# Kernel optimization log

Measured on AMD Instinct MI355X. Metric: run time of the kernel, lower is better.

Reference implementation:

```python
import jax, jax.numpy as jnp
import numpy as np

N_NODES = 100000
N_EDGES = 1000000
F_IN = 64
F_HID = 32


def setup_inputs() -> dict:
    key = jax.random.key(0)
    k = jax.random.split(key, 6)
    x = jax.random.normal(k[0], (N_NODES, F_IN), dtype=jnp.float32)
    edge_index = jax.random.randint(k[1], (2, N_EDGES), 0, N_NODES, dtype=jnp.int32)
    # Glorot-ish scaled weights (PyG GCNConv linear has no bias; bias added post-aggregation)
    W1 = jax.random.normal(k[2], (F_IN, F_HID), dtype=jnp.float32) / np.sqrt(F_IN)
    b1 = jax.random.normal(k[3], (F_HID,), dtype=jnp.float32) * 0.01
    W2 = jax.random.normal(k[4], (F_HID, F_IN), dtype=jnp.float32) / np.sqrt(F_HID)
    b2 = jax.random.normal(k[5], (F_IN,), dtype=jnp.float32) * 0.01
    return {"x": x, "edge_index": edge_index, "W1": W1, "b1": b1, "W2": W2, "b2": b2}


def gcn_conv(x, W, b, src, dst, n):
    """PyG GCNConv: h = x @ W; add self-loops; symmetric norm; scatter-add; + bias."""
    h = x @ W  # [N, out]
    ones = jnp.ones(src.shape[0], dtype=h.dtype)
    # degree includes the implicit self-loop (+1 per node)
    deg = jax.ops.segment_sum(ones, dst, num_segments=n) + 1.0  # [N]
    dis = jax.lax.rsqrt(deg)  # deg^{-1/2}
    norm = dis[src] * dis[dst]  # [E]
    agg = jax.ops.segment_sum(h[src] * norm[:, None], dst, num_segments=n)
    # self-loop contribution: norm_ii = deg_i^{-1}
    agg = agg + h * (dis * dis)[:, None]
    return agg + b


def reference(x, edge_index, W1, b1, W2, b2):
    src, dst = edge_index[0], edge_index[1]
    n = x.shape[0]
    h = jax.nn.relu(gcn_conv(x, W1, b1, src, dst, n))
    # dropout is identity in eval mode
    return gcn_conv(h, W2, b2, src, dst, n)
```

## Files before the change

kernel.cpp:

```cpp
#include <hip/hip_runtime.h>
#include <hip/hip_fp16.h>

#define NN 100000
#define NE 1000000
#define FIN 64
#define FHID 32
#define NB 782
#define BNODES 128
#define NCH 256
#define CH ((NE + NCH - 1) / NCH)
#define GEMB ((NN + 31) / 32)

union H8 { __half2 h2[4]; float4 f4; };
union H4 { __half2 h2[2]; float2 f2; };

__global__ __launch_bounds__(256) void k_bhist(const int* __restrict__ dst, int* __restrict__ phist) {
    __shared__ int lh[NB];
    for (int i = threadIdx.x; i < NB; i += 256) lh[i] = 0;
    __syncthreads();
    int k = blockIdx.x;
    int e0 = k * CH, e1 = min(e0 + CH, NE);
    for (int e = e0 + threadIdx.x; e < e1; e += 256) atomicAdd(&lh[dst[e] >> 7], 1);
    __syncthreads();
    for (int b = threadIdx.x; b < NB; b += 256) phist[(size_t)k * NB + b] = lh[b];
}

__global__ __launch_bounds__(256) void k_bscan(int* __restrict__ phist, int* __restrict__ btot) {
    int b = blockIdx.x;
    int k = threadIdx.x;
    int v = phist[(size_t)k * NB + b];
    int lane = k & 63, wv = k >> 6;
    int incl = v;
#pragma unroll
    for (int s = 1; s < 64; s <<= 1) {
        int t = __shfl_up(incl, s, 64);
        if (lane >= s) incl += t;
    }
    __shared__ int wt[4];
    if (lane == 63) wt[wv] = incl;
    __syncthreads();
    int add = 0;
#pragma unroll
    for (int w = 0; w < 4; ++w) add += (w < wv) ? wt[w] : 0;
    phist[(size_t)k * NB + b] = add + incl - v;
    if (k == 255) btot[b] = add + incl;
}

__global__ __launch_bounds__(1024) void k_bbase(const int* __restrict__ btot, int* __restrict__ bbase,
                                                int* __restrict__ off) {
    __shared__ int s[1024];
    int b = threadIdx.x;
    int v = (b < NB) ? btot[b] : 0;
    s[b] = v;
    __syncthreads();
    for (int d = 1; d < 1024; d <<= 1) {
        int t = (b >= d) ? s[b - d] : 0;
        __syncthreads();
        s[b] += t;
        __syncthreads();
    }
    if (b < NB) bbase[b] = s[b] - v;
    if (b == 0) { bbase[NB] = NE; off[NN] = NE; }
}

__global__ __launch_bounds__(256) void k_scatter_gemm1(const int* __restrict__ ei,
                                                       const int* __restrict__ phist,
                                                       const int* __restrict__ bbase,
                                                       int* __restrict__ ebuf,
                                                       const float* __restrict__ x,
                                                       const float* __restrict__ W1,
                                                       __half* __restrict__ h1) {
    int r = blockIdx.x;
    bool issc;
    int id;
    if (r < 2 * NCH) { issc = !(r & 1); id = r >> 1; }
    else             { issc = false;    id = r - NCH; }
    if (issc) {
        __shared__ int lh[NB];
        __shared__ int lbase[NB];
        int k = id;
        for (int b = threadIdx.x; b < NB; b += 256) {
            lh[b] = 0;
            lbase[b] = bbase[b] + phist[(size_t)k * NB + b];
        }
        __syncthreads();
        int e0 = k * CH, e1 = min(e0 + CH, NE);
        for (int e = e0 + threadIdx.x; e < e1; e += 256) {
            int s = ei[e], d = ei[NE + e];
            int bb = d >> 7;
            int rr = atomicAdd(&lh[bb], 1);
            ebuf[lbase[bb] + rr] = s * BNODES + (d & 127);
        }
        return;
    }
    __shared__ float Wl[FIN * FHID];
    for (int t = threadIdx.x; t < FIN * FHID / 4; t += 256)
        reinterpret_cast<float4*>(Wl)[t] = reinterpret_cast<const float4*>(W1)[t];
    __syncthreads();
    int row = id * 32 + (threadIdx.x >> 3);
    int l = threadIdx.x & 7;
    if (row >= NN) return;
    const float4* xr = reinterpret_cast<const float4*>(x + (size_t)row * FIN);
    float4 acc = make_float4(0.f, 0.f, 0.f, 0.f);
#pragma unroll
    for (int k4 = 0; k4 < FIN / 4; ++k4) {
        float4 a4 = xr[k4];
#pragma unroll
        for (int j = 0; j < 4; ++j) {
            float a = j == 0 ? a4.x : j == 1 ? a4.y : j == 2 ? a4.z : a4.w;
            const float4 wv = *reinterpret_cast<const float4*>(Wl + (k4 * 4 + j) * FHID + l * 4);
            acc.x += a * wv.x; acc.y += a * wv.y; acc.z += a * wv.z; acc.w += a * wv.w;
        }
    }
    H4 u;
    u.h2[0] = __floats2half2_rn(acc.x, acc.y);
    u.h2[1] = __floats2half2_rn(acc.z, acc.w);
    *reinterpret_cast<float2*>(h1 + (size_t)row * FHID + l * 4) = u.f2;
}

__global__ __launch_bounds__(256) void k_csr(const int* __restrict__ ebuf, const int* __restrict__ bbase,
                                             int* __restrict__ off, float* __restrict__ dis,
                                             int* __restrict__ csr) {
    __shared__ int nh[BNODES];
    __shared__ int ofl[BNODES];
    int b = blockIdx.x;
    int n0 = b * BNODES;
    int ebeg = bbase[b], eend = bbase[b + 1];
    int ld = threadIdx.x;
    if (ld < BNODES) nh[ld] = 0;
    __syncthreads();
    for (int e = ebeg + threadIdx.x; e < eend; e += 256) atomicAdd(&nh[ebuf[e] & 127], 1);
    __syncthreads();
    int dval = (ld < BNODES) ? nh[ld] : 0;
    if (ld < BNODES) ofl[ld] = dval;
    __syncthreads();
    for (int s = 1; s < BNODES; s <<= 1) {
        int t = 0;
        if (ld < BNODES && ld >= s) t = ofl[ld - s];
        __syncthreads();
        if (ld < BNODES) ofl[ld] += t;
        __syncthreads();
    }
    if (ld < BNODES) {
        ofl[ld] -= dval;
        int n = n0 + ld;
        if (n < NN) {
            off[n] = ebeg + ofl[ld];
            dis[n] = rsqrtf((float)dval + 1.0f);
        }
        nh[ld] = 0;
    }
    __syncthreads();
    for (int e = ebeg + threadIdx.x; e < eend; e += 256) {
        int v = ebuf[e];
        int ldd = v & 127;
        int r = atomicAdd(&nh[ldd], 1);
        csr[ebeg + ofl[ldd] + r] = v >> 7;
    }
}

__global__ __launch_bounds__(256) void k_gather1(const int* __restrict__ off, const int* __restrict__ csr,
                                                 const float* __restrict__ dis,
                                                 const __half* __restrict__ h, const float* __restrict__ bias,
                                                 __half* __restrict__ out) {
    int t = blockIdx.x * 256 + threadIdx.x;
    int n = t >> 4;
    int l = t & 15;
    int q = l >> 2, c = l & 3;
    float dn = dis[n];
    int beg = off[n], end = off[n + 1];
    float acc[8] = {0.f, 0.f, 0.f, 0.f, 0.f, 0.f, 0.f, 0.f};
    int p = beg + q;
    int s = (p < end) ? csr[p] : 0;
    for (; p < end; p += 4) {
        int scur = s;
        if (p + 4 < end) s = csr[p + 4];
        float nr = dis[scur] * dn;
        float4 v = *reinterpret_cast<const float4*>(h + (size_t)scur * FHID + c * 8);
        const __half2* hp = reinterpret_cast<const __half2*>(&v);
#pragma unroll
        for (int j = 0; j < 4; ++j) {
            float2 f = __half22float2(hp[j]);
            acc[2 * j] += f.x * nr;
            acc[2 * j + 1] += f.y * nr;
        }
    }
#pragma unroll
    for (int j = 0; j < 8; ++j) {
        acc[j] += __shfl_xor(acc[j], 4);
        acc[j] += __shfl_xor(acc[j], 8);
    }
    if (q == 0) {
        float d2 = dn * dn;
        float4 sv = *reinterpret_cast<const float4*>(h + (size_t)n * FHID + c * 8);
        const __half2* sp = reinterpret_cast<const __half2*>(&sv);
#pragma unroll
        for (int j = 0; j < 4; ++j) {
            float2 f = __half22float2(sp[j]);
            acc[2 * j] += f.x * d2;
            acc[2 * j + 1] += f.y * d2;
        }
        const float4 b0 = *reinterpret_cast<const float4*>(bias + c * 8);
        const float4 b1v = *reinterpret_cast<const float4*>(bias + c * 8 + 4);
        acc[0] += b0.x; acc[1] += b0.y; acc[2] += b0.z; acc[3] += b0.w;
        acc[4] += b1v.x; acc[5] += b1v.y; acc[6] += b1v.z; acc[7] += b1v.w;
#pragma unroll
        for (int j = 0; j < 8; ++j) acc[j] = acc[j] > 0.f ? acc[j] : 0.f;
        H8 o;
#pragma unroll
        for (int j = 0; j < 4; ++j) o.h2[j] = __floats2half2_rn(acc[2 * j], acc[2 * j + 1]);
        *reinterpret_cast<float4*>(out + (size_t)n * FHID + c * 8) = o.f4;
    }
}

__global__ __launch_bounds__(256) void k_gather_mm(const int* __restrict__ off, const int* __restrict__ csr,
                                                   const float* __restrict__ dis,
                                                   const __half* __restrict__ h, const float* __restrict__ W2,
                                                   const float* __restrict__ b2, float* __restrict__ out) {
    __shared__ float WL[FHID * FIN];
    __shared__ float aggL[16 * 36];
    for (int t = threadIdx.x; t < FHID * FIN / 4; t += 256)
        reinterpret_cast<float4*>(WL)[t] = reinterpret_cast<const float4*>(W2)[t];

    int i = threadIdx.x >> 4;
    int l = threadIdx.x & 15;
    int q = l >> 2, c = l & 3;
    int n = blockIdx.x * 16 + i;
    {
        float dn = dis[n];
        int beg = off[n], end = off[n + 1];
        float acc[8] = {0.f, 0.f, 0.f, 0.f, 0.f, 0.f, 0.f, 0.f};
        int p = beg + q;
        int s = (p < end) ? csr[p] : 0;
        for (; p < end; p += 4) {
            int scur = s;
            if (p + 4 < end) s = csr[p + 4];
            float nr = dis[scur] * dn;
            float4 v = *reinterpret_cast<const float4*>(h + (size_t)scur * FHID + c * 8);
            const __half2* hp = reinterpret_cast<const __half2*>(&v);
#pragma unroll
            for (int j = 0; j < 4; ++j) {
                float2 f = __half22float2(hp[j]);
                acc[2 * j] += f.x * nr;
                acc[2 * j + 1] += f.y * nr;
            }
        }
#pragma unroll
        for (int j = 0; j < 8; ++j) {
            acc[j] += __shfl_xor(acc[j], 4);
            acc[j] += __shfl_xor(acc[j], 8);
        }
        if (q == 0) {
            float d2 = dn * dn;
            float4 sv = *reinterpret_cast<const float4*>(h + (size_t)n * FHID + c * 8);
            const __half2* sp = reinterpret_cast<const __half2*>(&sv);
#pragma unroll
            for (int j = 0; j < 4; ++j) {
                float2 f = __half22float2(sp[j]);
                acc[2 * j] += f.x * d2;
                acc[2 * j + 1] += f.y * d2;
            }
            float* ar = aggL + i * 36 + c * 8;
            *reinterpret_cast<float4*>(ar) = make_float4(acc[0], acc[1], acc[2], acc[3]);
            *reinterpret_cast<float4*>(ar + 4) = make_float4(acc[4], acc[5], acc[6], acc[7]);
        }
    }
    __syncthreads();

    int r = threadIdx.x >> 4;
    int n2 = blockIdx.x * 16 + r;
    int c0 = (threadIdx.x & 15) * 4;
    float4 a0 = *reinterpret_cast<const float4*>(b2 + c0);
    const float* ag = aggL + r * 36;
#pragma unroll
    for (int k = 0; k < FHID; ++k) {
        float a = ag[k];
        const float4 wv = *reinterpret_cast<const float4*>(WL + k * FIN + c0);
        a0.x += a * wv.x; a0.y += a * wv.y; a0.z += a * wv.z; a0.w += a * wv.w;
    }
    *reinterpret_cast<float4*>(out + (size_t)n2 * FIN + c0) = a0;
}

extern "C" void kernel_launch(void* const* d_in, const int* in_sizes, int n_in,
                              void* d_out, int out_size, void* d_ws, size_t ws_size,
                              hipStream_t stream) {
    const float* x  = (const float*)d_in[0];
    const int*   ei = (const int*)d_in[1];
    const float* W1 = (const float*)d_in[2];
    const float* b1 = (const float*)d_in[3];
    const float* W2 = (const float*)d_in[4];
    const float* b2 = (const float*)d_in[5];
    float* out = (float*)d_out;

    char* w = (char*)d_ws;
    auto align = [](size_t v) { return (v + 255) & ~(size_t)255; };
    int*    phist = (int*)w;    w += align((size_t)NCH * NB * 4);
    int*    btot  = (int*)w;    w += align((size_t)NB * 4);
    int*    bbase = (int*)w;    w += align((size_t)(NB + 1) * 4);
    int*    ebuf  = (int*)w;    w += align((size_t)NE * 4);
    int*    off   = (int*)w;    w += align((size_t)(NN + 1) * 4);
    float*  dis   = (float*)w;  w += align((size_t)NN * 4);
    int*    csr   = (int*)w;    w += align((size_t)NE * 4);
    __half* h1    = (__half*)w; w += align((size_t)NN * FHID * 2);
    __half* hbuf  = (__half*)w; w += align((size_t)NN * FHID * 2);

    const int* dst = ei + NE;
    k_bhist<<<NCH, 256, 0, stream>>>(dst, phist);
    k_bscan<<<NB, 256, 0, stream>>>(phist, btot);
    k_bbase<<<1, 1024, 0, stream>>>(btot, bbase, off);
    k_scatter_gemm1<<<NCH + GEMB, 256, 0, stream>>>(ei, phist, bbase, ebuf, x, W1, h1);
    k_csr<<<NB, 256, 0, stream>>>(ebuf, bbase, off, dis, csr);
    k_gather1<<<(NN * 16) / 256, 256, 0, stream>>>(off, csr, dis, h1, b1, hbuf);
    k_gather_mm<<<NN / 16, 256, 0, stream>>>(off, csr, dis, hbuf, W2, b2, out);
}
```

Before: 95.03 us.

## Pre-scale features by source norm and widen gather to 32 lanes per node

Multiplies h1 rows by deg^-1/2 inside the CSR build kernel and folds the destination norm into the epilogue. Layer-1 output is likewise stored pre-scaled by dis. This removes the per-edge dis[src] gather and multiply from both aggregation loops. Each node now gets 32 lanes (8 edge streams) instead of 16, which raises memory-level parallelism but drops the csr index prefetch and doubles the block count. The extra read-modify-write of h1 in k_csr costs added traffic, and the scaled half values change rounding slightly.

```diff
diff --git a/kernel.cpp b/kernel.cpp
--- a/kernel.cpp
+++ b/kernel.cpp
@@ -120,9 +120,10 @@
 
 __global__ __launch_bounds__(256) void k_csr(const int* __restrict__ ebuf, const int* __restrict__ bbase,
                                              int* __restrict__ off, float* __restrict__ dis,
-                                             int* __restrict__ csr) {
+                                             int* __restrict__ csr, __half* __restrict__ h1) {
     __shared__ int nh[BNODES];
     __shared__ int ofl[BNODES];
+    __shared__ float sdis[BNODES];
     int b = blockIdx.x;
     int n0 = b * BNODES;
     int ebeg = bbase[b], eend = bbase[b + 1];
@@ -143,10 +144,12 @@
     }
     if (ld < BNODES) {
         ofl[ld] -= dval;
+        float dv = rsqrtf((float)dval + 1.0f);
+        sdis[ld] = dv;
         int n = n0 + ld;
         if (n < NN) {
             off[n] = ebeg + ofl[ld];
-            dis[n] = rsqrtf((float)dval + 1.0f);
+            dis[n] = dv;
         }
         nh[ld] = 0;
     }
@@ -157,6 +160,23 @@
         int r = atomicAdd(&nh[ldd], 1);
         csr[ebeg + ofl[ldd] + r] = v >> 7;
     }
+    int i = ld >> 1, part = ld & 1;
+    int n = n0 + i;
+    if (n < NN) {
+        float dv = sdis[i];
+        float4* pr = reinterpret_cast<float4*>(h1 + (size_t)n * FHID + part * 16);
+#pragma unroll
+        for (int j = 0; j < 2; ++j) {
+            float4 v4 = pr[j];
+            __half2* hp = reinterpret_cast<__half2*>(&v4);
+#pragma unroll
+            for (int u = 0; u < 4; ++u) {
+                float2 f = __half22float2(hp[u]);
+                hp[u] = __floats2half2_rn(f.x * dv, f.y * dv);
+            }
+            pr[j] = v4;
+        }
+    }
 }
 
 __global__ __launch_bounds__(256) void k_gather1(const int* __restrict__ off, const int* __restrict__ csr,
@@ -164,51 +184,50 @@
                                                  const __half* __restrict__ h, const float* __restrict__ bias,
                                                  __half* __restrict__ out) {
     int t = blockIdx.x * 256 + threadIdx.x;
-    int n = t >> 4;
-    int l = t & 15;
+    int n = t >> 5;
+    int l = t & 31;
     int q = l >> 2, c = l & 3;
     float dn = dis[n];
     int beg = off[n], end = off[n + 1];
     float acc[8] = {0.f, 0.f, 0.f, 0.f, 0.f, 0.f, 0.f, 0.f};
-    int p = beg + q;
-    int s = (p < end) ? csr[p] : 0;
-    for (; p < end; p += 4) {
-        int scur = s;
-        if (p + 4 < end) s = csr[p + 4];
-        float nr = dis[scur] * dn;
-        float4 v = *reinterpret_cast<const float4*>(h + (size_t)scur * FHID + c * 8);
+    for (int p = beg + q; p < end; p += 8) {
+        int s = csr[p];
+        float4 v = *reinterpret_cast<const float4*>(h + (size_t)s * FHID + c * 8);
         const __half2* hp = reinterpret_cast<const __half2*>(&v);
 #pragma unroll
         for (int j = 0; j < 4; ++j) {
             float2 f = __half22float2(hp[j]);
-            acc[2 * j] += f.x * nr;
-            acc[2 * j + 1] += f.y * nr;
+            acc[2 * j] += f.x;
+            acc[2 * j + 1] += f.y;
         }
     }
 #pragma unroll
     for (int j = 0; j < 8; ++j) {
         acc[j] += __shfl_xor(acc[j], 4);
         acc[j] += __shfl_xor(acc[j], 8);
+        acc[j] += __shfl_xor(acc[j], 16);
     }
     if (q == 0) {
-        float d2 = dn * dn;
         float4 sv = *reinterpret_cast<const float4*>(h + (size_t)n * FHID + c * 8);
         const __half2* sp = reinterpret_cast<const __half2*>(&sv);
 #pragma unroll
         for (int j = 0; j < 4; ++j) {
             float2 f = __half22float2(sp[j]);
-            acc[2 * j] += f.x * d2;
-            acc[2 * j + 1] += f.y * d2;
+            acc[2 * j] += f.x;
+            acc[2 * j + 1] += f.y;
         }
         const float4 b0 = *reinterpret_cast<const float4*>(bias + c * 8);
         const float4 b1v = *reinterpret_cast<const float4*>(bias + c * 8 + 4);
-        acc[0] += b0.x; acc[1] += b0.y; acc[2] += b0.z; acc[3] += b0.w;
-        acc[4] += b1v.x; acc[5] += b1v.y; acc[6] += b1v.z; acc[7] += b1v.w;
-#pragma unroll
-        for (int j = 0; j < 8; ++j) acc[j] = acc[j] > 0.f ? acc[j] : 0.f;
+        float bb[8] = {b0.x, b0.y, b0.z, b0.w, b1v.x, b1v.y, b1v.z, b1v.w};
         H8 o;
 #pragma unroll
-        for (int j = 0; j < 4; ++j) o.h2[j] = __floats2half2_rn(acc[2 * j], acc[2 * j + 1]);
+        for (int j = 0; j < 4; ++j) {
+            float v0 = dn * acc[2 * j] + bb[2 * j];
+            float v1 = dn * acc[2 * j + 1] + bb[2 * j + 1];
+            v0 = v0 > 0.f ? v0 : 0.f;
+            v1 = v1 > 0.f ? v1 : 0.f;
+            o.h2[j] = __floats2half2_rn(dn * v0, dn * v1);
+        }
         *reinterpret_cast<float4*>(out + (size_t)n * FHID + c * 8) = o.f4;
     }
 }
@@ -218,67 +237,62 @@
                                                    const __half* __restrict__ h, const float* __restrict__ W2,
                                                    const float* __restrict__ b2, float* __restrict__ out) {
     __shared__ float WL[FHID * FIN];
-    __shared__ float aggL[16 * 36];
+    __shared__ float aggL[8 * 36];
     for (int t = threadIdx.x; t < FHID * FIN / 4; t += 256)
         reinterpret_cast<float4*>(WL)[t] = reinterpret_cast<const float4*>(W2)[t];
 
-    int i = threadIdx.x >> 4;
-    int l = threadIdx.x & 15;
+    int i = threadIdx.x >> 5;
+    int l = threadIdx.x & 31;
     int q = l >> 2, c = l & 3;
-    int n = blockIdx.x * 16 + i;
+    int n = blockIdx.x * 8 + i;
     {
         float dn = dis[n];
         int beg = off[n], end = off[n + 1];
         float acc[8] = {0.f, 0.f, 0.f, 0.f, 0.f, 0.f, 0.f, 0.f};
-        int p = beg + q;
-        int s = (p < end) ? csr[p] : 0;
-        for (; p < end; p += 4) {
-            int scur = s;
-            if (p + 4 < end) s = csr[p + 4];
-            float nr = dis[scur] * dn;
-            float4 v = *reinterpret_cast<const float4*>(h + (size_t)scur * FHID + c * 8);
+        for (int p = beg + q; p < end; p += 8) {
+            int s = csr[p];
+            float4 v = *reinterpret_cast<const float4*>(h + (size_t)s * FHID + c * 8);
             const __half2* hp = reinterpret_cast<const __half2*>(&v);
 #pragma unroll
             for (int j = 0; j < 4; ++j) {
                 float2 f = __half22float2(hp[j]);
-                acc[2 * j] += f.x * nr;
-                acc[2 * j + 1] += f.y * nr;
+                acc[2 * j] += f.x;
+                acc[2 * j + 1] += f.y;
             }
         }
 #pragma unroll
         for (int j = 0; j < 8; ++j) {
             acc[j] += __shfl_xor(acc[j], 4);
             acc[j] += __shfl_xor(acc[j], 8);
+            acc[j] += __shfl_xor(acc[j], 16);
         }
         if (q == 0) {
-            float d2 = dn * dn;
             float4 sv = *reinterpret_cast<const float4*>(h + (size_t)n * FHID + c * 8);
             const __half2* sp = reinterpret_cast<const __half2*>(&sv);
+            float* ar = aggL + i * 36 + c * 8;
 #pragma unroll
             for (int j = 0; j < 4; ++j) {
                 float2 f = __half22float2(sp[j]);
-                acc[2 * j] += f.x * d2;
-                acc[2 * j + 1] += f.y * d2;
+                ar[2 * j] = dn * (acc[2 * j] + f.x);
+                ar[2 * j + 1] = dn * (acc[2 * j + 1] + f.y);
             }
-            float* ar = aggL + i * 36 + c * 8;
-            *reinterpret_cast<float4*>(ar) = make_float4(acc[0], acc[1], acc[2], acc[3]);
-            *reinterpret_cast<float4*>(ar + 4) = make_float4(acc[4], acc[5], acc[6], acc[7]);
-        }
-    }
-    __syncthreads();
-
-    int r = threadIdx.x >> 4;
-    int n2 = blockIdx.x * 16 + r;
-    int c0 = (threadIdx.x & 15) * 4;
-    float4 a0 = *reinterpret_cast<const float4*>(b2 + c0);
+        }
+    }
+    __syncthreads();
+
+    int r = threadIdx.x >> 5;
+    int n2 = blockIdx.x * 8 + r;
+    int cc = (threadIdx.x & 31) * 2;
+    float ax = b2[cc], ay = b2[cc + 1];
     const float* ag = aggL + r * 36;
 #pragma unroll
     for (int k = 0; k < FHID; ++k) {
         float a = ag[k];
-        const float4 wv = *reinterpret_cast<const float4*>(WL + k * FIN + c0);
-        a0.x += a * wv.x; a0.y += a * wv.y; a0.z += a * wv.z; a0.w += a * wv.w;
-    }
-    *reinterpret_cast<float4*>(out + (size_t)n2 * FIN + c0) = a0;
+        ax += a * WL[k * FIN + cc];
+        ay += a * WL[k * FIN + cc + 1];
+    }
+    float2 o2 = make_float2(ax, ay);
+    *reinterpret_cast<float2*>(out + (size_t)n2 * FIN + cc) = o2;
 }
 
 extern "C" void kernel_launch(void* const* d_in, const int* in_sizes, int n_in,
@@ -309,7 +323,7 @@
     k_bscan<<<NB, 256, 0, stream>>>(phist, btot);
     k_bbase<<<1, 1024, 0, stream>>>(btot, bbase, off);
     k_scatter_gemm1<<<NCH + GEMB, 256, 0, stream>>>(ei, phist, bbase, ebuf, x, W1, h1);
-    k_csr<<<NB, 256, 0, stream>>>(ebuf, bbase, off, dis, csr);
-    k_gather1<<<(NN * 16) / 256, 256, 0, stream>>>(off, csr, dis, h1, b1, hbuf);
-    k_gather_mm<<<NN / 16, 256, 0, stream>>>(off, csr, dis, hbuf, W2, b2, out);
-}
+    k_csr<<<NB, 256, 0, stream>>>(ebuf, bbase, off, dis, csr, h1);
+    k_gather1<<<(NN * 32) / 256, 256, 0, stream>>>(off, csr, dis, h1, b1, hbuf);
+    k_gather_mm<<<NN / 8, 256, 0, stream>>>(off, csr, dis, hbuf, W2, b2, out);
+}
```

Result: slower. 111.9 us (+17.7%).
